# Kernel optimization log

Measured on AMD Instinct MI355X. Metric: run time of the kernel, lower is better.

Reference implementation:

```python
import jax, jax.numpy as jnp
import numpy as np

# Fano-plane triples defining octonion multiplication: e_a e_b = e_c (cyclic)
_TRIPLES = [(1, 2, 4), (2, 3, 5), (3, 4, 6), (4, 5, 7), (5, 6, 1), (6, 7, 2), (7, 1, 3)]


def _oct_structure():
    """S3[i,j,k] = sign s.t. e_i * e_j = s * e_k (zero otherwise)."""
    idx = np.zeros((8, 8), dtype=np.int32)
    sgn = np.zeros((8, 8), dtype=np.float32)
    for j in range(8):
        idx[0, j] = j; sgn[0, j] = 1.0
    for i in range(1, 8):
        idx[i, 0] = i; sgn[i, 0] = 1.0
        idx[i, i] = 0; sgn[i, i] = -1.0
    for a, b, c in _TRIPLES:
        for (p, q, r) in ((a, b, c), (b, c, a), (c, a, b)):
            idx[p, q] = r; sgn[p, q] = 1.0
            idx[q, p] = r; sgn[q, p] = -1.0
    S3 = np.zeros((8, 8, 8), dtype=np.float32)
    for i in range(8):
        for j in range(8):
            S3[i, j, idx[i, j]] = sgn[i, j]
    return jnp.asarray(S3)


def _oct_full(W, S3):
    """Fold octonion structure into a dense block matrix.

    W: [8, out8, in8] per-component weights. Effective map:
      y_k = sum_{i,j} S3[i,j,k] * W_i @ x_j  ->  M[k*out8:, j*in8:] = sum_i S3[i,j,k] W_i
    Returns [8*out8, 8*in8].
    """
    M = jnp.einsum('ijk,ion->kojn', S3, W)  # [8, out8, 8, in8]
    k8, o8, j8, n8 = M.shape
    return M.reshape(k8 * o8, j8 * n8)


def setup_inputs() -> dict:
    key = jax.random.key(0)
    ks = jax.random.split(key, 6)
    B, T, D = 8, 1024, 1024
    S = 2048  # d_state = n_embd * expand_factor
    x = jax.random.normal(ks[0], (B, T, D), dtype=jnp.float32)
    h_prev = jnp.zeros((B, S), dtype=jnp.float32)
    WA = jax.random.normal(ks[1], (8, S // 8, S // 8), dtype=jnp.float32) * float(1.0 / np.sqrt(S))
    WB = jax.random.normal(ks[2], (8, S // 8, D // 8), dtype=jnp.float32) * float(1.0 / np.sqrt(D))
    WC = jax.random.normal(ks[3], (8, D // 8, S // 8), dtype=jnp.float32) * float(1.0 / np.sqrt(S))
    Wdelta = jax.random.normal(ks[4], (S, D), dtype=jnp.float32) * float(1.0 / np.sqrt(D))
    delta_bias = jnp.full((S,), -2.0, dtype=jnp.float32)
    return dict(x=x, h_prev=h_prev, WA=WA, WB=WB, WC=WC, Wdelta=Wdelta, delta_bias=delta_bias)


def reference(x, h_prev, WA, WB, WC, Wdelta, delta_bias):
    S3 = _oct_structure()
    Af = _oct_full(WA, S3)  # [S, S]
    Bf = _oct_full(WB, S3)  # [S, D]
    Cf = _oct_full(WC, S3)  # [D, S]
    # Selective gate: sigmoid(x @ Wdelta^T + bias)  [B, T, S]
    delta = jax.nn.sigmoid(jnp.einsum('btd,sd->bts', x, Wdelta) + delta_bias)
    # Input injection precomputed for all timesteps (B is time-invariant)
    Bx = jnp.einsum('btd,sd->bts', x, Bf)  # [B, T, S]

    def step(h, inp):
        bx_t, d_t = inp  # [B, S], [B, S]
        h_new = (1.0 - d_t) * h + d_t * (h @ Af.T + bx_t)
        return h_new, h_new

    h_last, hs = jax.lax.scan(step, h_prev, (jnp.swapaxes(Bx, 0, 1), jnp.swapaxes(delta, 0, 1)))
    # Readout applied to the full state history at once: y[t] = C(h[t])
    y = jnp.einsum('tbs,ds->btd', hs, Cf)  # [B, T, D]
    return y, h_last
```

## Files before the change

### kernel.cpp

```cpp
#include <hip/hip_runtime.h>
#include <hip/hip_bf16.h>

#define T_STEPS 1024
#define OFF_AFT   0ull
#define OFF_GCAT  4194304ull
#define OFF_CFT   8388608ull
#define OFF_DELTA 10485760ull
#define OFF_BX    27262976ull
#define OFF_HS    44040192ull
#define OFF_HBUF  60817408ull
#define OFF_CNT   60850176ull

typedef short short8 __attribute__((ext_vector_type(8)));
typedef float f32x4 __attribute__((ext_vector_type(4)));

__device__ __forceinline__ void build_oct_tables(int tid, int (*Is)[8], float (*Sg)[8]) {
  if (tid < 64) {
    int i = tid >> 3, j = tid & 7;
    int k = 0; float s = 0.f;
    if (i == 0)      { k = j; s = 1.f; }
    else if (j == 0) { k = i; s = 1.f; }
    else if (i == j) { k = 0; s = -1.f; }
    else {
      const int T7[7][3] = {{1,2,4},{2,3,5},{3,4,6},{4,5,7},{5,6,1},{6,7,2},{7,1,3}};
      for (int t = 0; t < 7; ++t) {
        int a = T7[t][0], b = T7[t][1], c = T7[t][2];
        const int P[3][3] = {{a,b,c},{b,c,a},{c,a,b}};
        for (int r = 0; r < 3; ++r) {
          if (i == P[r][0] && j == P[r][1]) { k = P[r][2]; s = 1.f; }
          if (i == P[r][1] && j == P[r][0]) { k = P[r][2]; s = -1.f; }
        }
      }
    }
    Is[j][k] = i; Sg[j][k] = s;
  }
  __syncthreads();
}

__device__ __forceinline__ unsigned short bf16r(float x) {
  unsigned u = __float_as_uint(x);
  return (unsigned short)((u + 0x7FFFu + ((u >> 16) & 1u)) >> 16);
}

__global__ __launch_bounds__(256) void fold_Ab(const float* __restrict__ WA, unsigned short* __restrict__ AfB) {
  __shared__ int Is[8][8]; __shared__ float Sg[8][8];
  build_oct_tables(threadIdx.x, Is, Sg);
  int g8 = blockIdx.x * 256 + threadIdx.x;
  int sp = g8 >> 8;
  int s0 = (g8 & 255) * 8;
  int k8 = sp >> 8, o = sp & 255;
  int j8 = s0 >> 8, n = s0 & 255;
  int i = Is[j8][k8]; float sg = Sg[j8][k8];
  const float* src = WA + (size_t)i * 65536 + (size_t)o * 256 + n;
  float4 f0 = *(const float4*)(src);
  float4 f1 = *(const float4*)(src + 4);
  unsigned short v[8];
  v[0] = bf16r(sg * f0.x); v[1] = bf16r(sg * f0.y); v[2] = bf16r(sg * f0.z); v[3] = bf16r(sg * f0.w);
  v[4] = bf16r(sg * f1.x); v[5] = bf16r(sg * f1.y); v[6] = bf16r(sg * f1.z); v[7] = bf16r(sg * f1.w);
  *(short8*)(AfB + (size_t)g8 * 8) = *(short8*)v;
}

__global__ __launch_bounds__(256) void fold_GC(const float* __restrict__ Wd, const float* __restrict__ WB,
                                               float* __restrict__ Gcat) {
  __shared__ int Is[8][8]; __shared__ float Sg[8][8];
  build_oct_tables(threadIdx.x, Is, Sg);
  int g4 = blockIdx.x * 256 + threadIdx.x;
  int col = (g4 & 1023) * 4;
  int d = g4 >> 10;
  float4 v;
  if (col < 2048) {
    v.x = Wd[(size_t)(col + 0) * 1024 + d];
    v.y = Wd[(size_t)(col + 1) * 1024 + d];
    v.z = Wd[(size_t)(col + 2) * 1024 + d];
    v.w = Wd[(size_t)(col + 3) * 1024 + d];
  } else {
    int sp = col - 2048;
    int k = sp >> 8;
    int j = d >> 7, n = d & 127;
    int i = Is[j][k]; float sg = Sg[j][k];
    const float* wb = WB + (size_t)i * 32768 + n;
    v.x = sg * wb[(size_t)((sp + 0) & 255) * 128];
    v.y = sg * wb[(size_t)((sp + 1) & 255) * 128];
    v.z = sg * wb[(size_t)((sp + 2) & 255) * 128];
    v.w = sg * wb[(size_t)((sp + 3) & 255) * 128];
  }
  *(float4*)(Gcat + (size_t)g4 * 4) = v;
}

__global__ __launch_bounds__(256) void fold_C(const float* __restrict__ WC, float* __restrict__ CfT) {
  __shared__ int Is[8][8]; __shared__ float Sg[8][8];
  build_oct_tables(threadIdx.x, Is, Sg);
  int g4 = blockIdx.x * 256 + threadIdx.x;
  int d0 = (g4 & 255) * 4;
  int s  = g4 >> 8;
  int j = s >> 8, n = s & 255;
  int k = d0 >> 7;
  int i = Is[j][k]; float sg = Sg[j][k];
  const float* wc = WC + (size_t)i * 32768 + n;
  float4 v;
  v.x = sg * wc[(size_t)((d0 + 0) & 127) * 256];
  v.y = sg * wc[(size_t)((d0 + 1) & 127) * 256];
  v.z = sg * wc[(size_t)((d0 + 2) & 127) * 256];
  v.w = sg * wc[(size_t)((d0 + 3) & 127) * 256];
  *(float4*)(CfT + (size_t)g4 * 4) = v;
}

__global__ __launch_bounds__(256) void init_h(const float* __restrict__ h_prev, unsigned long long* __restrict__ hx,
                                              int* __restrict__ cnt) {
  int gid = blockIdx.x * 256 + threadIdx.x;
  if (gid < 8192) {
    int c = gid >> 6, within = gid & 63;
    int pr = within >> 3, b = within & 7;
    int s = c * 16 + pr * 2;
    unsigned pk = (unsigned)bf16r(h_prev[(size_t)b * 2048 + s])
                | ((unsigned)bf16r(h_prev[(size_t)b * 2048 + s + 1]) << 16);
    hx[gid] = ((unsigned long long)pk << 32) | 0ull;
  } else {
    hx[gid] = 0x00000000FFFFFFFFull;
  }
  if (gid < 32) cnt[gid] = 0;
}

__global__ __launch_bounds__(512) void scan_dbx_y(const unsigned short* __restrict__ AfB,
                                                  float* __restrict__ dlt, float* __restrict__ Bx,
                                                  float* __restrict__ hs,
                                                  unsigned long long* __restrict__ hx,
                                                  const float* __restrict__ h_prev, float* __restrict__ hlast,
                                                  const float* __restrict__ X, const float* __restrict__ G,
                                                  const float* __restrict__ bias,
                                                  const float* __restrict__ CfT, float* __restrict__ out,
                                                  int* __restrict__ chunkCnt, int* __restrict__ scanProg) {
  __shared__ __attribute__((aligned(16))) unsigned short Sm[4 * 128 * 40];
  const int bid = blockIdx.x;
  const int tid = threadIdx.x;
  const int lane = tid & 63;

  if (bid >= 2176) {
    const int gi = bid - 2176;
    const int ck = gi >> 6;
    const int idx = gi & 63;
    const int bm = (idx >> 3) * 8 + ck;
    const int bn = idx & 7;
    if (tid == 0) {
      while (__hip_atomic_load(&scanProg[ck], __ATOMIC_RELAXED, __HIP_MEMORY_SCOPE_SYSTEM) < 128)
        __builtin_amdgcn_s_sleep(32);
    }
    __syncthreads();
    unsigned short* As = Sm;
    unsigned short* Bs = Sm + 128 * 40;
    const int w8 = tid >> 6;
    const int wr = w8 >> 2, wc = w8 & 3;
    const int lr = lane & 15, lk = lane >> 4;

    f32x4 acc[4][2];
    #pragma unroll
    for (int a = 0; a < 4; ++a) { acc[a][0] = (f32x4){0.f,0.f,0.f,0.f}; acc[a][1] = (f32x4){0.f,0.f,0.f,0.f}; }

    for (int kt = 0; kt < 2048; kt += 32) {
      {
        int row = tid >> 2, kq = tid & 3;
        int rg = bm * 128 + row;
        const float* ar = hs + (size_t)((rg & 1023) * 8 + (rg >> 10)) * 2048 + kt + kq * 8;
        float4 f0 = *(const float4*)(ar);
        float4 f1 = *(const float4*)(ar + 4);
        float vv[8] = {f0.x, f0.y, f0.z, f0.w, f1.x, f1.y, f1.z, f1.w};
        unsigned* a32 = (unsigned*)As + row * 20 + kq * 4;
        #pragma unroll
        for (int j = 0; j < 4; ++j)
          a32[j] = (unsigned)bf16r(vv[2 * j]) | ((unsigned)bf16r(vv[2 * j + 1]) << 16);
      }
      {
        int kr = tid >> 4, cg = tid & 15;
        const float* br = CfT + (size_t)(kt + kr) * 1024 + bn * 128 + cg * 8;
        float4 f0 = *(const float4*)(br);
        float4 f1 = *(const float4*)(br + 4);
        float vv[8] = {f0.x, f0.y, f0.z, f0.w, f1.x, f1.y, f1.z, f1.w};
        #pragma unroll
        for (int e = 0; e < 8; ++e)
          Bs[(cg * 8 + e) * 40 + kr] = bf16r(vv[e]);
      }
      __syncthreads();
      short8 aF[4], bF[2];
      #pragma unroll
      for (int f = 0; f < 4; ++f)
        aF[f] = *(const short8*)(As + (wr * 64 + f * 16 + lr) * 40 + lk * 8);
      #pragma unroll
      for (int e = 0; e < 2; ++e)
        bF[e] = *(const short8*)(Bs + (wc * 32 + e * 16 + lr) * 40 + lk * 8);
      #pragma unroll
      for (int fm = 0; fm < 4; ++fm)
        #pragma unroll
        for (int fn = 0; fn < 2; ++fn)
          acc[fm][fn] = __builtin_amdgcn_mfma_f32_16x16x32_bf16(aF[fm], bF[fn], acc[fm][fn], 0, 0, 0);
      __syncthreads();
    }
    #pragma unroll
    for (int fm = 0; fm < 4; ++fm)
      #pragma unroll
      for (int rr = 0; rr < 4; ++rr) {
        size_t rg = bm * 128 + wr * 64 + fm * 16 + lk * 4 + rr;
        #pragma unroll
        for (int fn = 0; fn < 2; ++fn) {
          int n = bn * 128 + wc * 32 + fn * 16 + lr;
          out[rg * 1024 + n] = acc[fm][fn][rr];
        }
      }
    return;
  }

  if (bid >= 128) {
    const int gi = bid - 128;
    const int bn = gi & 31;
    const int bmSeq = gi >> 5;
    const int ck = bmSeq >> 3, bb = bmSeq & 7;
    const int bm = ck + 8 * bb;
    unsigned short* Ah = Sm;
    unsigned short* Al = Ah + 128 * 40;
    unsigned short* Bh = Al + 128 * 40;
    unsigned short* Bl = Bh + 128 * 40;
    const int w8 = tid >> 6;
    const int wr = w8 >> 2, wc = w8 & 3;
    const int lr = lane & 15, lk = lane >> 4;

    f32x4 acc[4][2];
    #pragma unroll
    for (int a = 0; a < 4; ++a) { acc[a][0] = (f32x4){0.f,0.f,0.f,0.f}; acc[a][1] = (f32x4){0.f,0.f,0.f,0.f}; }

    for (int kt = 0; kt < 1024; kt += 32) {
      {
        int row = tid >> 2, kq = tid & 3;
        const float* ar = X + (size_t)(bm * 128 + row) * 1024 + kt + kq * 8;
        float4 f0 = *(const float4*)(ar);
        float4 f1 = *(const float4*)(ar + 4);
        float vv[8] = {f0.x, f0.y, f0.z, f0.w, f1.x, f1.y, f1.z, f1.w};
        unsigned* ah32 = (unsigned*)Ah + row * 20 + kq * 4;
        unsigned* al32 = (unsigned*)Al + row * 20 + kq * 4;
        #pragma unroll
        for (int j = 0; j < 4; ++j) {
          unsigned short h0 = bf16r(vv[2 * j]), h1 = bf16r(vv[2 * j + 1]);
          float r0 = vv[2 * j]     - __uint_as_float((unsigned)h0 << 16);
          float r1 = vv[2 * j + 1] - __uint_as_float((unsigned)h1 << 16);
          ah32[j] = (unsigned)h0 | ((unsigned)h1 << 16);
          al32[j] = (unsigned)bf16r(r0) | ((unsigned)bf16r(r1) << 16);
        }
      }
      {
        int kr = tid >> 4, cg = tid & 15;
        const float* br = G + (size_t)(kt + kr) * 4096 + bn * 128 + cg * 8;
        float4 f0 = *(const float4*)(br);
        float4 f1 = *(const float4*)(br + 4);
        float vv[8] = {f0.x, f0.y, f0.z, f0.w, f1.x, f1.y, f1.z, f1.w};
        #pragma unroll
        for (int e = 0; e < 8; ++e) {
          int n = cg * 8 + e;
          unsigned short h = bf16r(vv[e]);
          float r = vv[e] - __uint_as_float((unsigned)h << 16);
          Bh[n * 40 + kr] = h;
          Bl[n * 40 + kr] = bf16r(r);
        }
      }
      __syncthreads();
      short8 ahf[4], alf[4], bhf[2], blf[2];
      #pragma unroll
      for (int f = 0; f < 4; ++f) {
        int ma = (wr * 64 + f * 16 + lr) * 40 + lk * 8;
        ahf[f] = *(const short8*)(Ah + ma);
        alf[f] = *(const short8*)(Al + ma);
      }
      #pragma unroll
      for (int e = 0; e < 2; ++e) {
        int nb2 = (wc * 32 + e * 16 + lr) * 40 + lk * 8;
        bhf[e] = *(const short8*)(Bh + nb2);
        blf[e] = *(const short8*)(Bl + nb2);
      }
      #pragma unroll
      for (int fm = 0; fm < 4; ++fm)
        #pragma unroll
        for (int fn = 0; fn < 2; ++fn) {
          acc[fm][fn] = __builtin_amdgcn_mfma_f32_16x16x32_bf16(ahf[fm], bhf[fn], acc[fm][fn], 0, 0, 0);
          acc[fm][fn] = __builtin_amdgcn_mfma_f32_16x16x32_bf16(ahf[fm], blf[fn], acc[fm][fn], 0, 0, 0);
          acc[fm][fn] = __builtin_amdgcn_mfma_f32_16x16x32_bf16(alf[fm], bhf[fn], acc[fm][fn], 0, 0, 0);
        }
      __syncthreads();
    }
    const bool isDelta = (bn < 16);
    #pragma unroll
    for (int fm = 0; fm < 4; ++fm) {
      #pragma unroll
      for (int rr = 0; rr < 4; ++rr) {
        int r = bm * 128 + wr * 64 + fm * 16 + lk * 4 + rr;
        int t = r & 1023, b = r >> 10;
        size_t base = ((size_t)t * 8 + b) * 2048;
        #pragma unroll
        for (int fn = 0; fn < 2; ++fn) {
          int n = bn * 128 + wc * 32 + fn * 16 + lr;
          float v = acc[fm][fn][rr];
          if (isDelta) {
            v += bias[n];
            v = 1.0f / (1.0f + expf(-v));
            __hip_atomic_store(&dlt[base + n], v, __ATOMIC_RELAXED, __HIP_MEMORY_SCOPE_SYSTEM);
          } else {
            __hip_atomic_store(&Bx[base + (n - 2048)], v, __ATOMIC_RELAXED, __HIP_MEMORY_SCOPE_SYSTEM);
          }
        }
      }
    }
    __syncthreads();
    if (tid == 0)
      __hip_atomic_fetch_add(&chunkCnt[ck], 1, __ATOMIC_RELAXED, __HIP_MEMORY_SCOPE_SYSTEM);
    return;
  }

  float* red = (float*)Sm;
  const int wg = bid;
  const int w = tid >> 6;
  const int row = lane & 15;
  const int g4 = lane >> 4;
  const int nb = lane & 7;

  short8 afr[8];
  {
    const unsigned short* ab = AfB + (size_t)(wg * 16 + row) * 2048 + w * 256 + g4 * 8;
    #pragma unroll
    for (int q = 0; q < 8; ++q)
      afr[q] = *(const short8*)(ab + q * 32);
  }
  const int S0 = (g4 & 1) * 32 + nb;

  const int ub = tid >> 3, usp = (tid & 7) * 2;
  const int pword = wg * 64 + (tid & 7) * 8 + ub;
  float hr0 = 0.f, hr1 = 0.f;
  if (tid < 64) {
    hr0 = h_prev[(size_t)ub * 2048 + wg * 16 + usp];
    hr1 = h_prev[(size_t)ub * 2048 + wg * 16 + usp + 1];
  }

  #pragma unroll 1
  for (int t = 0; t < T_STEPS; ++t) {
    float2 dv = make_float2(0.f, 0.f), bxv = make_float2(0.f, 0.f);
    if (tid < 64) {
      if ((t & 127) == 0) {
        const int ck = t >> 7;
        while (__hip_atomic_load(&chunkCnt[ck], __ATOMIC_RELAXED, __HIP_MEMORY_SCOPE_SYSTEM) < 256)
          __builtin_amdgcn_s_sleep(16);
      }
      size_t off = ((size_t)t * 8 + ub) * 2048 + wg * 16 + usp;
      dv  = *(const float2*)(dlt + off);
      bxv = *(const float2*)(Bx + off);
    }
    const unsigned want = (unsigned)t;
    const unsigned long long* bq = hx + (size_t)(t & 1) * 8192 + (size_t)w * 1024 + lane;
    unsigned long long wv[16];
    #pragma unroll
    for (int p = 0; p < 16; ++p)
      wv[p] = __hip_atomic_load(bq + p * 64, __ATOMIC_RELAXED, __HIP_MEMORY_SCOPE_SYSTEM);
    int fails = 0;
    for (;;) {
      bool stale = false;
      #pragma unroll
      for (int p = 0; p < 16; ++p) stale |= ((unsigned)wv[p] != want);
      if (!__any(stale)) break;
      if (++fails > 4) __builtin_amdgcn_s_sleep(1);
      #pragma unroll
      for (int p = 0; p < 16; ++p)
        if ((unsigned)wv[p] != want)
          wv[p] = __hip_atomic_load(bq + p * 64, __ATOMIC_RELAXED, __HIP_MEMORY_SCOPE_SYSTEM);
    }
    unsigned hi[16];
    #pragma unroll
    for (int p = 0; p < 16; ++p) hi[p] = (unsigned)(wv[p] >> 32);

    f32x4 acc = {0.f, 0.f, 0.f, 0.f};
    #pragma unroll
    for (int q = 0; q < 8; ++q) {
      union { unsigned d[4]; short8 v; } bb;
      #pragma unroll
      for (int u = 0; u < 4; ++u) {
        int S = S0 + u * 8;
        unsigned c0 = __shfl(hi[2 * q],     S, 64);
        unsigned c1 = __shfl(hi[2 * q + 1], S, 64);
        bb.d[u] = (g4 & 2) ? c1 : c0;
      }
      acc = __builtin_amdgcn_mfma_f32_16x16x32_bf16(afr[q], bb.v, acc, 0, 0, 0);
    }
    float* rb = &red[(t & 1) * 1152];
    if (row < 8) {
      #pragma unroll
      for (int r = 0; r < 4; ++r)
        rb[w * 144 + (g4 * 4 + r) * 9 + row] = acc[r];
    }
    __syncthreads();
    if (tid < 64) {
      __builtin_amdgcn_s_setprio(1);
      float o0 = 0.f, o1 = 0.f;
      #pragma unroll
      for (int ww = 0; ww < 8; ++ww) {
        o0 += rb[ww * 144 + usp * 9 + ub];
        o1 += rb[ww * 144 + (usp + 1) * 9 + ub];
      }
      float h0 = fmaf(dv.x, o0 + bxv.x - hr0, hr0);
      float h1 = fmaf(dv.y, o1 + bxv.y - hr1, hr1);
      hr0 = h0; hr1 = h1;
      unsigned pk = (unsigned)bf16r(h0) | ((unsigned)bf16r(h1) << 16);
      unsigned long long wval = ((unsigned long long)pk << 32) | (unsigned long long)(unsigned)(t + 1);
      __hip_atomic_store(hx + (size_t)((t + 1) & 1) * 8192 + pword, wval,
                         __ATOMIC_RELAXED, __HIP_MEMORY_SCOPE_SYSTEM);
      __builtin_amdgcn_s_setprio(0);
      size_t off = ((size_t)t * 8 + ub) * 2048 + wg * 16 + usp;
      union { float2 f; unsigned long long u; } hsv; hsv.f = make_float2(h0, h1);
      __hip_atomic_store((unsigned long long*)(hs + off), hsv.u,
                         __ATOMIC_RELAXED, __HIP_MEMORY_SCOPE_SYSTEM);
      if (t == T_STEPS - 1)
        *(float2*)(hlast + (size_t)ub * 2048 + wg * 16 + usp) = make_float2(h0, h1);
      if ((t & 127) == 127) {
        asm volatile("s_waitcnt vmcnt(0)" ::: "memory");
        if (tid == 0)
          __hip_atomic_fetch_add(&scanProg[t >> 7], 1, __ATOMIC_RELAXED, __HIP_MEMORY_SCOPE_SYSTEM);
      }
    }
  }
}

extern "C" void kernel_launch(void* const* d_in, const int* in_sizes, int n_in,
                              void* d_out, int out_size, void* d_ws, size_t ws_size,
                              hipStream_t stream) {
  const float* x      = (const float*)d_in[0];
  const float* h_prev = (const float*)d_in[1];
  const float* WA     = (const float*)d_in[2];
  const float* WB     = (const float*)d_in[3];
  const float* WC     = (const float*)d_in[4];
  const float* Wd     = (const float*)d_in[5];
  const float* bias   = (const float*)d_in[6];
  float* out = (float*)d_out;
  float* w = (float*)d_ws;
  unsigned short* AfB = (unsigned short*)(w + OFF_AFT);
  float* Gcat = w + OFF_GCAT;
  float* CfT  = w + OFF_CFT;
  float* dlt  = w + OFF_DELTA;
  float* Bx   = w + OFF_BX;
  float* hs   = w + OFF_HS;
  unsigned long long* hx = (unsigned long long*)(w + OFF_HBUF);
  int* chunkCnt = (int*)(w + OFF_CNT);
  int* scanProg = chunkCnt + 16;

  fold_Ab<<<2048, 256, 0, stream>>>(WA, AfB);
  fold_GC<<<4096, 256, 0, stream>>>(Wd, WB, Gcat);
  fold_C <<<2048, 256, 0, stream>>>(WC, CfT);
  init_h <<<64,   256, 0, stream>>>(h_prev, hx, chunkCnt);
  scan_dbx_y<<<2688, 512, 0, stream>>>(AfB, dlt, Bx, hs, hx, h_prev, out + 8388608,
                                       x, Gcat, bias, CfT, out, chunkCnt, scanProg);
}
```

Baseline: 4.184 ms.

## Split output GEMM out of scan kernel and merge fold launches

Removes the fused y-readout GEMM blocks, which polled per-chunk progress counters to overlap with the recurrent scan, and runs them instead as a separate gemm_y kernel after the scan. The four setup kernels (fold A, fold G/B, fold C, init_h) become one launch. Inside the scan, hs is written with a plain store instead of a system-scope atomic, and the double-buffered reduction area becomes single-buffered with an extra barrier each step. This cuts the spinning blocks, their atomics and launch overhead. It gives up overlapping the readout GEMM with the latency-bound scan and adds a per-step sync.

```diff
diff --git a/kernel.cpp b/kernel.cpp
--- a/kernel.cpp
+++ b/kernel.cpp
@@ -42,171 +42,92 @@
   return (unsigned short)((u + 0x7FFFu + ((u >> 16) & 1u)) >> 16);
 }
 
-__global__ __launch_bounds__(256) void fold_Ab(const float* __restrict__ WA, unsigned short* __restrict__ AfB) {
+__global__ __launch_bounds__(256) void fold_all(const float* __restrict__ WA, const float* __restrict__ WB,
+                                                const float* __restrict__ WC, const float* __restrict__ Wd,
+                                                const float* __restrict__ h_prev,
+                                                unsigned short* __restrict__ AfB, float* __restrict__ Gcat,
+                                                float* __restrict__ CfT, unsigned long long* __restrict__ hx,
+                                                int* __restrict__ cnt) {
   __shared__ int Is[8][8]; __shared__ float Sg[8][8];
   build_oct_tables(threadIdx.x, Is, Sg);
-  int g8 = blockIdx.x * 256 + threadIdx.x;
-  int sp = g8 >> 8;
-  int s0 = (g8 & 255) * 8;
-  int k8 = sp >> 8, o = sp & 255;
-  int j8 = s0 >> 8, n = s0 & 255;
-  int i = Is[j8][k8]; float sg = Sg[j8][k8];
-  const float* src = WA + (size_t)i * 65536 + (size_t)o * 256 + n;
-  float4 f0 = *(const float4*)(src);
-  float4 f1 = *(const float4*)(src + 4);
-  unsigned short v[8];
-  v[0] = bf16r(sg * f0.x); v[1] = bf16r(sg * f0.y); v[2] = bf16r(sg * f0.z); v[3] = bf16r(sg * f0.w);
-  v[4] = bf16r(sg * f1.x); v[5] = bf16r(sg * f1.y); v[6] = bf16r(sg * f1.z); v[7] = bf16r(sg * f1.w);
-  *(short8*)(AfB + (size_t)g8 * 8) = *(short8*)v;
-}
-
-__global__ __launch_bounds__(256) void fold_GC(const float* __restrict__ Wd, const float* __restrict__ WB,
-                                               float* __restrict__ Gcat) {
-  __shared__ int Is[8][8]; __shared__ float Sg[8][8];
-  build_oct_tables(threadIdx.x, Is, Sg);
-  int g4 = blockIdx.x * 256 + threadIdx.x;
-  int col = (g4 & 1023) * 4;
-  int d = g4 >> 10;
-  float4 v;
-  if (col < 2048) {
-    v.x = Wd[(size_t)(col + 0) * 1024 + d];
-    v.y = Wd[(size_t)(col + 1) * 1024 + d];
-    v.z = Wd[(size_t)(col + 2) * 1024 + d];
-    v.w = Wd[(size_t)(col + 3) * 1024 + d];
+  const int bid = blockIdx.x;
+  if (bid < 2048) {
+    int g8 = bid * 256 + threadIdx.x;
+    int sp = g8 >> 8;
+    int s0 = (g8 & 255) * 8;
+    int k8 = sp >> 8, o = sp & 255;
+    int j8 = s0 >> 8, n = s0 & 255;
+    int i = Is[j8][k8]; float sg = Sg[j8][k8];
+    const float* src = WA + (size_t)i * 65536 + (size_t)o * 256 + n;
+    float4 f0 = *(const float4*)(src);
+    float4 f1 = *(const float4*)(src + 4);
+    unsigned short v[8];
+    v[0] = bf16r(sg * f0.x); v[1] = bf16r(sg * f0.y); v[2] = bf16r(sg * f0.z); v[3] = bf16r(sg * f0.w);
+    v[4] = bf16r(sg * f1.x); v[5] = bf16r(sg * f1.y); v[6] = bf16r(sg * f1.z); v[7] = bf16r(sg * f1.w);
+    *(short8*)(AfB + (size_t)g8 * 8) = *(short8*)v;
+  } else if (bid < 6144) {
+    int g4 = (bid - 2048) * 256 + threadIdx.x;
+    int col = (g4 & 1023) * 4;
+    int d = g4 >> 10;
+    float4 v;
+    if (col < 2048) {
+      v.x = Wd[(size_t)(col + 0) * 1024 + d];
+      v.y = Wd[(size_t)(col + 1) * 1024 + d];
+      v.z = Wd[(size_t)(col + 2) * 1024 + d];
+      v.w = Wd[(size_t)(col + 3) * 1024 + d];
+    } else {
+      int sp = col - 2048;
+      int k = sp >> 8;
+      int j = d >> 7, n = d & 127;
+      int i = Is[j][k]; float sg = Sg[j][k];
+      const float* wb = WB + (size_t)i * 32768 + n;
+      v.x = sg * wb[(size_t)((sp + 0) & 255) * 128];
+      v.y = sg * wb[(size_t)((sp + 1) & 255) * 128];
+      v.z = sg * wb[(size_t)((sp + 2) & 255) * 128];
+      v.w = sg * wb[(size_t)((sp + 3) & 255) * 128];
+    }
+    *(float4*)(Gcat + (size_t)g4 * 4) = v;
+  } else if (bid < 8192) {
+    int g4 = (bid - 6144) * 256 + threadIdx.x;
+    int d0 = (g4 & 255) * 4;
+    int s  = g4 >> 8;
+    int j = s >> 8, n = s & 255;
+    int k = d0 >> 7;
+    int i = Is[j][k]; float sg = Sg[j][k];
+    const float* wc = WC + (size_t)i * 32768 + n;
+    float4 v;
+    v.x = sg * wc[(size_t)((d0 + 0) & 127) * 256];
+    v.y = sg * wc[(size_t)((d0 + 1) & 127) * 256];
+    v.z = sg * wc[(size_t)((d0 + 2) & 127) * 256];
+    v.w = sg * wc[(size_t)((d0 + 3) & 127) * 256];
+    *(float4*)(CfT + (size_t)g4 * 4) = v;
   } else {
-    int sp = col - 2048;
-    int k = sp >> 8;
-    int j = d >> 7, n = d & 127;
-    int i = Is[j][k]; float sg = Sg[j][k];
-    const float* wb = WB + (size_t)i * 32768 + n;
-    v.x = sg * wb[(size_t)((sp + 0) & 255) * 128];
-    v.y = sg * wb[(size_t)((sp + 1) & 255) * 128];
-    v.z = sg * wb[(size_t)((sp + 2) & 255) * 128];
-    v.w = sg * wb[(size_t)((sp + 3) & 255) * 128];
-  }
-  *(float4*)(Gcat + (size_t)g4 * 4) = v;
-}
-
-__global__ __launch_bounds__(256) void fold_C(const float* __restrict__ WC, float* __restrict__ CfT) {
-  __shared__ int Is[8][8]; __shared__ float Sg[8][8];
-  build_oct_tables(threadIdx.x, Is, Sg);
-  int g4 = blockIdx.x * 256 + threadIdx.x;
-  int d0 = (g4 & 255) * 4;
-  int s  = g4 >> 8;
-  int j = s >> 8, n = s & 255;
-  int k = d0 >> 7;
-  int i = Is[j][k]; float sg = Sg[j][k];
-  const float* wc = WC + (size_t)i * 32768 + n;
-  float4 v;
-  v.x = sg * wc[(size_t)((d0 + 0) & 127) * 256];
-  v.y = sg * wc[(size_t)((d0 + 1) & 127) * 256];
-  v.z = sg * wc[(size_t)((d0 + 2) & 127) * 256];
-  v.w = sg * wc[(size_t)((d0 + 3) & 127) * 256];
-  *(float4*)(CfT + (size_t)g4 * 4) = v;
-}
-
-__global__ __launch_bounds__(256) void init_h(const float* __restrict__ h_prev, unsigned long long* __restrict__ hx,
-                                              int* __restrict__ cnt) {
-  int gid = blockIdx.x * 256 + threadIdx.x;
-  if (gid < 8192) {
-    int c = gid >> 6, within = gid & 63;
-    int pr = within >> 3, b = within & 7;
-    int s = c * 16 + pr * 2;
-    unsigned pk = (unsigned)bf16r(h_prev[(size_t)b * 2048 + s])
-                | ((unsigned)bf16r(h_prev[(size_t)b * 2048 + s + 1]) << 16);
-    hx[gid] = ((unsigned long long)pk << 32) | 0ull;
-  } else {
-    hx[gid] = 0x00000000FFFFFFFFull;
-  }
-  if (gid < 32) cnt[gid] = 0;
-}
-
-__global__ __launch_bounds__(512) void scan_dbx_y(const unsigned short* __restrict__ AfB,
-                                                  float* __restrict__ dlt, float* __restrict__ Bx,
-                                                  float* __restrict__ hs,
-                                                  unsigned long long* __restrict__ hx,
-                                                  const float* __restrict__ h_prev, float* __restrict__ hlast,
-                                                  const float* __restrict__ X, const float* __restrict__ G,
-                                                  const float* __restrict__ bias,
-                                                  const float* __restrict__ CfT, float* __restrict__ out,
-                                                  int* __restrict__ chunkCnt, int* __restrict__ scanProg) {
+    int gid = (bid - 8192) * 256 + threadIdx.x;
+    if (gid < 8192) {
+      int c = gid >> 6, within = gid & 63;
+      int pr = within >> 3, b = within & 7;
+      int s = c * 16 + pr * 2;
+      unsigned pk = (unsigned)bf16r(h_prev[(size_t)b * 2048 + s])
+                  | ((unsigned)bf16r(h_prev[(size_t)b * 2048 + s + 1]) << 16);
+      hx[gid] = ((unsigned long long)pk << 32) | 0ull;
+    } else {
+      hx[gid] = 0x00000000FFFFFFFFull;
+    }
+    if (gid < 16) cnt[gid] = 0;
+  }
+}
+
+__global__ __launch_bounds__(512) void scan_dbx(const unsigned short* __restrict__ AfB,
+                                                float* __restrict__ dlt, float* __restrict__ Bx,
+                                                float* __restrict__ hs,
+                                                unsigned long long* __restrict__ hx,
+                                                const float* __restrict__ h_prev, float* __restrict__ hlast,
+                                                const float* __restrict__ X, const float* __restrict__ G,
+                                                const float* __restrict__ bias, int* __restrict__ chunkCnt) {
   __shared__ __attribute__((aligned(16))) unsigned short Sm[4 * 128 * 40];
   const int bid = blockIdx.x;
   const int tid = threadIdx.x;
   const int lane = tid & 63;
-
-  if (bid >= 2176) {
-    const int gi = bid - 2176;
-    const int ck = gi >> 6;
-    const int idx = gi & 63;
-    const int bm = (idx >> 3) * 8 + ck;
-    const int bn = idx & 7;
-    if (tid == 0) {
-      while (__hip_atomic_load(&scanProg[ck], __ATOMIC_RELAXED, __HIP_MEMORY_SCOPE_SYSTEM) < 128)
-        __builtin_amdgcn_s_sleep(32);
-    }
-    __syncthreads();
-    unsigned short* As = Sm;
-    unsigned short* Bs = Sm + 128 * 40;
-    const int w8 = tid >> 6;
-    const int wr = w8 >> 2, wc = w8 & 3;
-    const int lr = lane & 15, lk = lane >> 4;
-
-    f32x4 acc[4][2];
-    #pragma unroll
-    for (int a = 0; a < 4; ++a) { acc[a][0] = (f32x4){0.f,0.f,0.f,0.f}; acc[a][1] = (f32x4){0.f,0.f,0.f,0.f}; }
-
-    for (int kt = 0; kt < 2048; kt += 32) {
-      {
-        int row = tid >> 2, kq = tid & 3;
-        int rg = bm * 128 + row;
-        const float* ar = hs + (size_t)((rg & 1023) * 8 + (rg >> 10)) * 2048 + kt + kq * 8;
-        float4 f0 = *(const float4*)(ar);
-        float4 f1 = *(const float4*)(ar + 4);
-        float vv[8] = {f0.x, f0.y, f0.z, f0.w, f1.x, f1.y, f1.z, f1.w};
-        unsigned* a32 = (unsigned*)As + row * 20 + kq * 4;
-        #pragma unroll
-        for (int j = 0; j < 4; ++j)
-          a32[j] = (unsigned)bf16r(vv[2 * j]) | ((unsigned)bf16r(vv[2 * j + 1]) << 16);
-      }
-      {
-        int kr = tid >> 4, cg = tid & 15;
-        const float* br = CfT + (size_t)(kt + kr) * 1024 + bn * 128 + cg * 8;
-        float4 f0 = *(const float4*)(br);
-        float4 f1 = *(const float4*)(br + 4);
-        float vv[8] = {f0.x, f0.y, f0.z, f0.w, f1.x, f1.y, f1.z, f1.w};
-        #pragma unroll
-        for (int e = 0; e < 8; ++e)
-          Bs[(cg * 8 + e) * 40 + kr] = bf16r(vv[e]);
-      }
-      __syncthreads();
-      short8 aF[4], bF[2];
-      #pragma unroll
-      for (int f = 0; f < 4; ++f)
-        aF[f] = *(const short8*)(As + (wr * 64 + f * 16 + lr) * 40 + lk * 8);
-      #pragma unroll
-      for (int e = 0; e < 2; ++e)
-        bF[e] = *(const short8*)(Bs + (wc * 32 + e * 16 + lr) * 40 + lk * 8);
-      #pragma unroll
-      for (int fm = 0; fm < 4; ++fm)
-        #pragma unroll
-        for (int fn = 0; fn < 2; ++fn)
-          acc[fm][fn] = __builtin_amdgcn_mfma_f32_16x16x32_bf16(aF[fm], bF[fn], acc[fm][fn], 0, 0, 0);
-      __syncthreads();
-    }
-    #pragma unroll
-    for (int fm = 0; fm < 4; ++fm)
-      #pragma unroll
-      for (int rr = 0; rr < 4; ++rr) {
-        size_t rg = bm * 128 + wr * 64 + fm * 16 + lk * 4 + rr;
-        #pragma unroll
-        for (int fn = 0; fn < 2; ++fn) {
-          int n = bn * 128 + wc * 32 + fn * 16 + lr;
-          out[rg * 1024 + n] = acc[fm][fn][rr];
-        }
-      }
-    return;
-  }
 
   if (bid >= 128) {
     const int gi = bid - 128;
@@ -383,11 +304,10 @@
       }
       acc = __builtin_amdgcn_mfma_f32_16x16x32_bf16(afr[q], bb.v, acc, 0, 0, 0);
     }
-    float* rb = &red[(t & 1) * 1152];
     if (row < 8) {
       #pragma unroll
       for (int r = 0; r < 4; ++r)
-        rb[w * 144 + (g4 * 4 + r) * 9 + row] = acc[r];
+        red[w * 144 + (g4 * 4 + r) * 9 + row] = acc[r];
     }
     __syncthreads();
     if (tid < 64) {
@@ -395,8 +315,8 @@
       float o0 = 0.f, o1 = 0.f;
       #pragma unroll
       for (int ww = 0; ww < 8; ++ww) {
-        o0 += rb[ww * 144 + usp * 9 + ub];
-        o1 += rb[ww * 144 + (usp + 1) * 9 + ub];
+        o0 += red[ww * 144 + usp * 9 + ub];
+        o1 += red[ww * 144 + (usp + 1) * 9 + ub];
       }
       float h0 = fmaf(dv.x, o0 + bxv.x - hr0, hr0);
       float h1 = fmaf(dv.y, o1 + bxv.y - hr1, hr1);
@@ -407,18 +327,79 @@
                          __ATOMIC_RELAXED, __HIP_MEMORY_SCOPE_SYSTEM);
       __builtin_amdgcn_s_setprio(0);
       size_t off = ((size_t)t * 8 + ub) * 2048 + wg * 16 + usp;
-      union { float2 f; unsigned long long u; } hsv; hsv.f = make_float2(h0, h1);
-      __hip_atomic_store((unsigned long long*)(hs + off), hsv.u,
-                         __ATOMIC_RELAXED, __HIP_MEMORY_SCOPE_SYSTEM);
+      *(float2*)(hs + off) = make_float2(h0, h1);
       if (t == T_STEPS - 1)
         *(float2*)(hlast + (size_t)ub * 2048 + wg * 16 + usp) = make_float2(h0, h1);
-      if ((t & 127) == 127) {
-        asm volatile("s_waitcnt vmcnt(0)" ::: "memory");
-        if (tid == 0)
-          __hip_atomic_fetch_add(&scanProg[t >> 7], 1, __ATOMIC_RELAXED, __HIP_MEMORY_SCOPE_SYSTEM);
-      }
-    }
-  }
+    }
+    __syncthreads();
+  }
+}
+
+__global__ __launch_bounds__(512) void gemm_y(const float* __restrict__ HS, const float* __restrict__ CfT,
+                                              float* __restrict__ out) {
+  __shared__ __attribute__((aligned(16))) unsigned short Sm[2 * 128 * 40];
+  unsigned short* As = Sm;
+  unsigned short* Bs = Sm + 128 * 40;
+  const int bn = blockIdx.x, bm = blockIdx.y;
+  const int tid = threadIdx.x;
+  const int lane = tid & 63;
+  const int w8 = tid >> 6;
+  const int wr = w8 >> 2, wc = w8 & 3;
+  const int lr = lane & 15, lk = lane >> 4;
+
+  f32x4 acc[4][2];
+  #pragma unroll
+  for (int a = 0; a < 4; ++a) { acc[a][0] = (f32x4){0.f,0.f,0.f,0.f}; acc[a][1] = (f32x4){0.f,0.f,0.f,0.f}; }
+
+  for (int kt = 0; kt < 2048; kt += 32) {
+    {
+      int row = tid >> 2, kq = tid & 3;
+      int rg = bm * 128 + row;
+      const float* ar = HS + (size_t)((rg & 1023) * 8 + (rg >> 10)) * 2048 + kt + kq * 8;
+      float4 f0 = *(const float4*)(ar);
+      float4 f1 = *(const float4*)(ar + 4);
+      float vv[8] = {f0.x, f0.y, f0.z, f0.w, f1.x, f1.y, f1.z, f1.w};
+      unsigned* a32 = (unsigned*)As + row * 20 + kq * 4;
+      #pragma unroll
+      for (int j = 0; j < 4; ++j)
+        a32[j] = (unsigned)bf16r(vv[2 * j]) | ((unsigned)bf16r(vv[2 * j + 1]) << 16);
+    }
+    {
+      int kr = tid >> 4, cg = tid & 15;
+      const float* br = CfT + (size_t)(kt + kr) * 1024 + bn * 128 + cg * 8;
+      float4 f0 = *(const float4*)(br);
+      float4 f1 = *(const float4*)(br + 4);
+      float vv[8] = {f0.x, f0.y, f0.z, f0.w, f1.x, f1.y, f1.z, f1.w};
+      #pragma unroll
+      for (int e = 0; e < 8; ++e)
+        Bs[(cg * 8 + e) * 40 + kr] = bf16r(vv[e]);
+    }
+    __syncthreads();
+    short8 aF[4], bF[2];
+    #pragma unroll
+    for (int f = 0; f < 4; ++f)
+      aF[f] = *(const short8*)(As + (wr * 64 + f * 16 + lr) * 40 + lk * 8);
+    #pragma unroll
+    for (int e = 0; e < 2; ++e)
+      bF[e] = *(const short8*)(Bs + (wc * 32 + e * 16 + lr) * 40 + lk * 8);
+    #pragma unroll
+    for (int fm = 0; fm < 4; ++fm)
+      #pragma unroll
+      for (int fn = 0; fn < 2; ++fn)
+        acc[fm][fn] = __builtin_amdgcn_mfma_f32_16x16x32_bf16(aF[fm], bF[fn], acc[fm][fn], 0, 0, 0);
+    __syncthreads();
+  }
+  #pragma unroll
+  for (int fm = 0; fm < 4; ++fm)
+    #pragma unroll
+    for (int rr = 0; rr < 4; ++rr) {
+      size_t rg = bm * 128 + wr * 64 + fm * 16 + lk * 4 + rr;
+      #pragma unroll
+      for (int fn = 0; fn < 2; ++fn) {
+        int n = bn * 128 + wc * 32 + fn * 16 + lr;
+        out[rg * 1024 + n] = acc[fm][fn][rr];
+      }
+    }
 }
 
 extern "C" void kernel_launch(void* const* d_in, const int* in_sizes, int n_in,
@@ -441,12 +422,9 @@
   float* hs   = w + OFF_HS;
   unsigned long long* hx = (unsigned long long*)(w + OFF_HBUF);
   int* chunkCnt = (int*)(w + OFF_CNT);
-  int* scanProg = chunkCnt + 16;
-
-  fold_Ab<<<2048, 256, 0, stream>>>(WA, AfB);
-  fold_GC<<<4096, 256, 0, stream>>>(Wd, WB, Gcat);
-  fold_C <<<2048, 256, 0, stream>>>(WC, CfT);
-  init_h <<<64,   256, 0, stream>>>(h_prev, hx, chunkCnt);
-  scan_dbx_y<<<2688, 512, 0, stream>>>(AfB, dlt, Bx, hs, hx, h_prev, out + 8388608,
-                                       x, Gcat, bias, CfT, out, chunkCnt, scanProg);
-}
+
+  fold_all<<<8256, 256, 0, stream>>>(WA, WB, WC, Wd, h_prev, AfB, Gcat, CfT, hx, chunkCnt);
+  scan_dbx<<<2176, 512, 0, stream>>>(AfB, dlt, Bx, hs, hx, h_prev, out + 8388608,
+                                     x, Gcat, bias, chunkCnt);
+  gemm_y<<<dim3(8, 64), 512, 0, stream>>>(hs, CfT, out);
+}
```

New measurement: 3.745 ms. 10.5% less time.
